# Optimization experiments

Measured on AMD Instinct MI355X. Metric: run time of the kernel, lower is better.

The kernel has to match this reference:

```python
import jax, jax.numpy as jnp
import numpy as np
import math

D = 768      # hidden_size
DK = 128     # d = min(128, hidden)
REL_K = 5
POS_RANGE = 2 * REL_K + 1
SCALING = math.sqrt(2 * DK)
LN_EPS = 1e-5


def setup_inputs() -> dict:
    key = jax.random.key(0)
    ks = jax.random.split(key, 16)
    N, S = 8, 2048
    sequence = jax.random.normal(ks[0], (N, S, D), dtype=jnp.float32)
    attention_mask = jnp.ones((N, S, S), dtype=bool)
    positions = jnp.tile(jnp.arange(S, dtype=jnp.int64)[None, :], (N, 1))
    s = 0.02
    params = dict(
        W_init=jax.random.normal(ks[1], (D, D), jnp.float32) * s,
        b_init=jnp.zeros((D,), jnp.float32),
        ln_g=jnp.ones((D,), jnp.float32),
        ln_b=jnp.zeros((D,), jnp.float32),
        W_u=jax.random.normal(ks[2], (D, 2 * D), jnp.float32) * s,
        b_u=jnp.zeros((2 * D,), jnp.float32),
        W_v=jax.random.normal(ks[3], (D, 2 * D), jnp.float32) * s,
        b_v=jnp.zeros((2 * D,), jnp.float32),
        W_z=jax.random.normal(ks[4], (D, DK), jnp.float32) * s,
        b_z=jnp.zeros((DK,), jnp.float32),
        gamma=jax.random.normal(ks[5], (3, DK), jnp.float32) * 0.02 + 0.0,
        beta=jnp.zeros((3, DK), jnp.float32),
        embed_pos=jax.random.normal(ks[6], (POS_RANGE, DK), jnp.float32),
        W_out=jax.random.normal(ks[7], (2 * D, D), jnp.float32) * s,
        b_out=jnp.zeros((D,), jnp.float32),
        W_gate=jax.random.normal(ks[8], (2 * D, D), jnp.float32) * s,
        b_gate=jnp.zeros((D,), jnp.float32),
    )
    return dict(sequence=sequence, attention_mask=attention_mask, positions=positions, **params)


def _layernorm(x, g, b):
    mu = jnp.mean(x, axis=-1, keepdims=True)
    var = jnp.mean(jnp.square(x - mu), axis=-1, keepdims=True)
    return (x - mu) * jax.lax.rsqrt(var + LN_EPS) * g + b


def reference(sequence, attention_mask, positions,
              W_init, b_init, ln_g, ln_b,
              W_u, b_u, W_v, b_v, W_z, b_z,
              gamma, beta, embed_pos,
              W_out, b_out, W_gate, b_gate):
    res = sequence
    x = _layernorm(sequence @ W_init + b_init, ln_g, ln_b)   # [N,S,D]
    U = jax.nn.silu(x @ W_u + b_u)                            # [N,S,2D]
    V = jax.nn.silu(x @ W_v + b_v)                            # [N,S,2D]
    Z = jax.nn.silu(x @ W_z + b_z)                            # [N,S,dk]
    Q = Z * gamma[0] + beta[0]
    Qp = Z * gamma[1] + beta[1]
    K = Z * gamma[2] + beta[2]
    energy = jnp.einsum('nsd,ntd->nst', Q, K)                 # [N,S,S]
    # relative position bias: Qp projected onto position embeddings,
    # then gathered by clipped relative offset (equivalent to one-hot+sum)
    q_pos = Qp @ embed_pos.T                                  # [N,S,pos_range]
    rel = positions[:, None, :] - positions[:, :, None]       # [N,S,S] = pos_j - pos_i
    rel_idx = jnp.clip(rel, -REL_K, REL_K) + REL_K
    rel_energy = jnp.take_along_axis(q_pos, rel_idx, axis=2)  # [N,S,S]
    logits = (energy + rel_energy) / SCALING
    logits = jnp.where(attention_mask, logits, -jnp.inf)
    attn = jax.nn.softmax(logits, axis=-1)
    V_ = jnp.einsum('nst,ntd->nsd', attn, V)                  # [N,S,2D]
    out = (U * V_) @ W_out + b_out                            # [N,S,D] (dropout inactive at eval)
    gates = jax.nn.sigmoid(jnp.concatenate([out, res], axis=-1) @ W_gate + b_gate)
    out = gates * out + (1.0 - gates) * res
    return out
```

## Files before the change

kernel.cpp:

```cpp
#include <hip/hip_runtime.h>
#include <math.h>


typedef __bf16 bf16x8 __attribute__((ext_vector_type(8)));
typedef float  f32x4  __attribute__((ext_vector_type(4)));

__device__ __forceinline__ float silu_f(float v) { return v / (1.0f + __expf(-v)); }
__device__ __forceinline__ float sigmoid_f(float v) { return 1.0f / (1.0f + __expf(-v)); }

__device__ __forceinline__ unsigned short f2bf(float f) {
    union { float f; unsigned u; } v; v.f = f;
    unsigned r = v.u + 0x7fff + ((v.u >> 16) & 1);
    return (unsigned short)(r >> 16);
}
__device__ __forceinline__ float bf2f(unsigned short h) {
    union { unsigned u; float f; } v; v.u = ((unsigned)h) << 16; return v.f;
}

__device__ __forceinline__ void gload_lds16(const void* g, void* l) {
    __builtin_amdgcn_global_load_lds((const __attribute__((address_space(1))) char*)g,
                                     (__attribute__((address_space(3))) char*)l, 16, 0, 0);
}

template <int EPI, bool DUAL>
__global__ __launch_bounds__(256) void mfma_gemm(
    const unsigned short* __restrict__ A,  int lda, long sA,
    const unsigned short* __restrict__ Bt, int ldb, long sB,
    const unsigned short* __restrict__ A2,
    const unsigned short* __restrict__ Bt2,
    const float* __restrict__ bias,
    const float* __restrict__ aux, long sAux,
    float* __restrict__ aux2,
    void* __restrict__ P0, long sP0,
    void* __restrict__ P1,
    int N, int K)
{
    __shared__ unsigned short As[128 * 64];
    __shared__ unsigned short Bs[128 * 64];
    const int tid  = threadIdx.x;
    const int lane = tid & 63;
    const int wave = tid >> 6;
    const int z    = blockIdx.z;
    const int row0 = blockIdx.y * 128;
    const int col0 = blockIdx.x * 128;

    int c_r[4], c_g[4];
    unsigned short* alp[4];
    unsigned short* blp[4];
#pragma unroll
    for (int ci = 0; ci < 4; ++ci) {
        const int c = ci * 256 + tid;
        const int r = c >> 3;
        c_r[ci] = r;
        c_g[ci] = (c & 7) ^ (r & 7);
        alp[ci] = &As[c * 8];
        blp[ci] = &Bs[c * 8];
    }

    const int wr = (wave >> 1) * 64;
    const int wc = (wave & 1) * 64;
    const int fm  = lane & 15;
    const int kbi = lane >> 4;
    const int er  = kbi * 4;

    int aoff[2][4], boff[2][4];
#pragma unroll
    for (int b = 0; b < 2; ++b)
#pragma unroll
        for (int i = 0; i < 4; ++i) {
            const int r = wr + i * 16 + fm;
            aoff[b][i] = r * 64 + (((b * 4 + kbi) ^ (r & 7)) * 8);
            const int n = wc + i * 16 + fm;
            boff[b][i] = n * 64 + (((b * 4 + kbi) ^ (n & 7)) * 8);
        }

    f32x4 acc[4][4];
#pragma unroll
    for (int i = 0; i < 4; ++i)
#pragma unroll
        for (int j = 0; j < 4; ++j) acc[i][j] = (f32x4){0.f, 0.f, 0.f, 0.f};

    const int npass = DUAL ? 2 : 1;
    for (int pass = 0; pass < npass; ++pass) {
        const unsigned short* Ab = (pass ? A2  : A)  + (size_t)z * sA;
        const unsigned short* Bb = (pass ? Bt2 : Bt) + (size_t)z * sB;
        const unsigned short* ag[4];
        const unsigned short* bg[4];
#pragma unroll
        for (int ci = 0; ci < 4; ++ci) {
            ag[ci] = Ab + (size_t)(row0 + c_r[ci]) * lda + c_g[ci] * 8;
            bg[ci] = Bb + (size_t)(col0 + c_r[ci]) * ldb + c_g[ci] * 8;
        }
        for (int k0 = 0; k0 < K; k0 += 64) {
#pragma unroll
            for (int ci = 0; ci < 4; ++ci) { gload_lds16(ag[ci], alp[ci]); ag[ci] += 64; }
#pragma unroll
            for (int ci = 0; ci < 4; ++ci) { gload_lds16(bg[ci], blp[ci]); bg[ci] += 64; }
            __syncthreads();
#pragma unroll
            for (int b = 0; b < 2; ++b) {
                bf16x8 a[4], bb[4];
#pragma unroll
                for (int i = 0; i < 4; ++i) a[i]  = *(const bf16x8*)&As[aoff[b][i]];
#pragma unroll
                for (int j = 0; j < 4; ++j) bb[j] = *(const bf16x8*)&Bs[boff[b][j]];
#pragma unroll
                for (int i = 0; i < 4; ++i)
#pragma unroll
                    for (int j = 0; j < 4; ++j)
                        acc[i][j] = __builtin_amdgcn_mfma_f32_16x16x32_bf16(
                            a[i], bb[j], acc[i][j], 0, 0, 0);
            }
            __syncthreads();
        }
    }

    if (EPI == 0) {
        unsigned short* Ub = (unsigned short*)P0 + (size_t)z * sP0;
        const float* inv = aux2 + (z << 11);
#pragma unroll
        for (int i = 0; i < 4; ++i)
#pragma unroll
            for (int j = 0; j < 4; ++j) {
                const int m0 = row0 + wr + i * 16 + er;
                const int n  = col0 + wc + j * 16 + fm;
#pragma unroll
                for (int reg = 0; reg < 4; ++reg) {
                    const size_t idx = (size_t)(m0 + reg) * N + n;
                    Ub[idx] = f2bf(acc[i][j][reg] * inv[m0 + reg] * bf2f(Ub[idx]));
                }
            }
    } else if (EPI == 1) {
        const float* qb = aux + (size_t)z * sAux;
        unsigned short* Eb = (unsigned short*)P0 + (size_t)z * sP0;
#pragma unroll
        for (int i = 0; i < 4; ++i) {
            float rs[4] = {0.f, 0.f, 0.f, 0.f};
#pragma unroll
            for (int j = 0; j < 4; ++j) {
                const int n = col0 + wc + j * 16 + fm;
#pragma unroll
                for (int reg = 0; reg < 4; ++reg) {
                    const int m = row0 + wr + i * 16 + er + reg;
                    int d = n - m;
                    d = d < -5 ? -5 : (d > 5 ? 5 : d);
                    const float v =
                        __expf((acc[i][j][reg] + qb[m * 11 + d + 5]) * 0.0625f);
                    const unsigned short h = f2bf(v);
                    Eb[(size_t)m * N + n] = h;
                    rs[reg] += bf2f(h);
                }
            }
#pragma unroll
            for (int reg = 0; reg < 4; ++reg) {
                float s = rs[reg];
                s += __shfl_xor(s, 1); s += __shfl_xor(s, 2);
                s += __shfl_xor(s, 4); s += __shfl_xor(s, 8);
                if (fm == 0) {
                    const int m = row0 + wr + i * 16 + er + reg;
                    aux2[((size_t)(z * 2048 + m)) * 32 + blockIdx.x * 2 + (wave & 1)] = s;
                }
            }
        }
    } else if (EPI == 2) {
        unsigned short* Cb = (unsigned short*)P0;
#pragma unroll
        for (int j = 0; j < 4; ++j) {
            const int n = col0 + wc + j * 16 + fm;
            const float bb = bias[n];
#pragma unroll
            for (int i = 0; i < 4; ++i) {
                const int m0 = row0 + wr + i * 16 + er;
#pragma unroll
                for (int reg = 0; reg < 4; ++reg)
                    Cb[(size_t)(m0 + reg) * N + n] = f2bf(acc[i][j][reg] + bb);
            }
        }
    } else if (EPI == 5) {
        float* Zf = (float*)P0;
#pragma unroll
        for (int j = 0; j < 4; ++j) {
            const int n = col0 + wc + j * 16 + fm;
            const float bb = bias[n];
#pragma unroll
            for (int i = 0; i < 4; ++i) {
                const int m0 = row0 + wr + i * 16 + er;
#pragma unroll
                for (int reg = 0; reg < 4; ++reg)
                    Zf[(size_t)(m0 + reg) * N + n] = silu_f(acc[i][j][reg] + bb);
            }
        }
    } else if (EPI == 6) {
        float* Of = (float*)P0;
        unsigned short* Ob = (unsigned short*)P1;
#pragma unroll
        for (int j = 0; j < 4; ++j) {
            const int n = col0 + wc + j * 16 + fm;
            const float bb = bias[n];
#pragma unroll
            for (int i = 0; i < 4; ++i) {
                const int m0 = row0 + wr + i * 16 + er;
#pragma unroll
                for (int reg = 0; reg < 4; ++reg) {
                    const float v = acc[i][j][reg] + bb;
                    const size_t idx = (size_t)(m0 + reg) * N + n;
                    Of[idx] = v;
                    Ob[idx] = f2bf(v);
                }
            }
        }
    } else if (EPI == 7) {
        float* Of = (float*)P0;
        const float* res = aux;
#pragma unroll
        for (int j = 0; j < 4; ++j) {
            const int n = col0 + wc + j * 16 + fm;
            const float bb = bias[n];
#pragma unroll
            for (int i = 0; i < 4; ++i) {
                const int m0 = row0 + wr + i * 16 + er;
#pragma unroll
                for (int reg = 0; reg < 4; ++reg) {
                    const float g = sigmoid_f(acc[i][j][reg] + bb);
                    const size_t idx = (size_t)(m0 + reg) * N + n;
                    Of[idx] = g * Of[idx] + (1.0f - g) * res[idx];
                }
            }
        }
    } else {
        unsigned short* Ub = (unsigned short*)P0;
        unsigned short* Vt = (unsigned short*)P1;
#pragma unroll
        for (int j = 0; j < 4; ++j) {
            const int n = col0 + wc + j * 16 + fm;
            const bool isU = n < 1536;
            const float bb = isU ? bias[n] : aux2[n - 1536];
#pragma unroll
            for (int i = 0; i < 4; ++i) {
                const int m0 = row0 + wr + i * 16 + er;
                if (isU) {
#pragma unroll
                    for (int reg = 0; reg < 4; ++reg)
                        Ub[(size_t)(m0 + reg) * 1536 + n] =
                            f2bf(silu_f(acc[i][j][reg] + bb));
                } else {
                    const int bat = m0 >> 11;
                    const int sl  = m0 & 2047;
                    unsigned short t[4];
#pragma unroll
                    for (int reg = 0; reg < 4; ++reg)
                        t[reg] = f2bf(silu_f(acc[i][j][reg] + bb));
                    *(ushort4*)(Vt + (size_t)bat * 1536 * 2048
                                + (size_t)(n - 1536) * 2048 + sl) = *(const ushort4*)t;
                }
            }
        }
    }
}

__global__ __launch_bounds__(256) void reduce_inv(
    const float* __restrict__ part, float* __restrict__ inv)
{
    const int r = blockIdx.x * 256 + threadIdx.x;
    const float4* p = (const float4*)(part + (size_t)r * 32);
    float s = 0.f;
#pragma unroll
    for (int k = 0; k < 8; ++k) {
        float4 v = p[k];
        s += v.x + v.y + v.z + v.w;
    }
    inv[r] = 1.0f / s;
}

__global__ __launch_bounds__(256) void transpose_w(
    const float* __restrict__ W, unsigned short* __restrict__ Wt, int K, int N)
{
    __shared__ float t[32][33];
    const int tx = threadIdx.x & 31, ty = threadIdx.x >> 5;
    const int kb = blockIdx.y * 32, nb = blockIdx.x * 32;
#pragma unroll
    for (int r = 0; r < 4; ++r)
        t[ty + 8 * r][tx] = W[(size_t)(kb + ty + 8 * r) * N + nb + tx];
    __syncthreads();
#pragma unroll
    for (int r = 0; r < 4; ++r)
        Wt[(size_t)(nb + ty + 8 * r) * K + kb + tx] = f2bf(t[tx][ty + 8 * r]);
}

__global__ __launch_bounds__(256) void f32_to_bf16(
    const float* __restrict__ in, unsigned short* __restrict__ o)
{
    const size_t i = ((size_t)blockIdx.x * 256 + threadIdx.x) * 4;
    float4 v = *(const float4*)(in + i);
    ushort4 b;
    b.x = f2bf(v.x); b.y = f2bf(v.y); b.z = f2bf(v.z); b.w = f2bf(v.w);
    *(ushort4*)(o + i) = b;
}

__global__ __launch_bounds__(256) void ln_bf16(
    const unsigned short* __restrict__ in, const float* __restrict__ g,
    const float* __restrict__ b, unsigned short* __restrict__ out)
{
    const int row = blockIdx.x;
    const unsigned short* p = in + (size_t)row * 768;
    const int tid = threadIdx.x;
    float v0 = bf2f(p[tid]), v1 = bf2f(p[tid + 256]), v2 = bf2f(p[tid + 512]);
    float s = v0 + v1 + v2;
    float q = v0 * v0 + v1 * v1 + v2 * v2;
#pragma unroll
    for (int off = 32; off; off >>= 1) {
        s += __shfl_xor(s, off);
        q += __shfl_xor(q, off);
    }
    __shared__ float ss[4], qq[4];
    const int wid = tid >> 6, lane = tid & 63;
    if (lane == 0) { ss[wid] = s; qq[wid] = q; }
    __syncthreads();
    s = ss[0] + ss[1] + ss[2] + ss[3];
    q = qq[0] + qq[1] + qq[2] + qq[3];
    const float mu  = s * (1.0f / 768.0f);
    const float var = q * (1.0f / 768.0f) - mu * mu;
    const float inv = rsqrtf(var + 1e-5f);
    unsigned short* o = out + (size_t)row * 768;
    o[tid]       = f2bf((v0 - mu) * inv * g[tid]       + b[tid]);
    o[tid + 256] = f2bf((v1 - mu) * inv * g[tid + 256] + b[tid + 256]);
    o[tid + 512] = f2bf((v2 - mu) * inv * g[tid + 512] + b[tid + 512]);
}

__global__ __launch_bounds__(256) void qpos_kernel(
    const float* __restrict__ Z, const float* __restrict__ g1,
    const float* __restrict__ b1, const float* __restrict__ ep,
    float* __restrict__ qpos)
{
    const int tid = threadIdx.x;
    const int lane = tid & 63;
    const int wid = tid >> 6;
    const int row = blockIdx.x * 4 + wid;
    const float z0 = Z[(size_t)row * 128 + lane];
    const float z1 = Z[(size_t)row * 128 + 64 + lane];
    const float q0 = z0 * g1[lane] + b1[lane];
    const float q1 = z1 * g1[64 + lane] + b1[64 + lane];
#pragma unroll
    for (int p = 0; p < 11; ++p) {
        float s = q0 * ep[p * 128 + lane] + q1 * ep[p * 128 + 64 + lane];
#pragma unroll
        for (int off = 32; off; off >>= 1) s += __shfl_xor(s, off);
        if (lane == 0) qpos[(size_t)row * 11 + p] = s;
    }
}

__global__ __launch_bounds__(256) void qk_affine(
    const float* __restrict__ Z, const float* __restrict__ gamma,
    const float* __restrict__ beta,
    unsigned short* __restrict__ Qb, unsigned short* __restrict__ Kb)
{
    const int idx = blockIdx.x * 256 + threadIdx.x;
    const int row = idx >> 5;
    const int c   = (idx & 31) * 4;
    float4 z  = *(const float4*)(Z + (size_t)row * 128 + c);
    float4 g0 = *(const float4*)(gamma + c);
    float4 B0 = *(const float4*)(beta + c);
    float4 g2 = *(const float4*)(gamma + 256 + c);
    float4 B2 = *(const float4*)(beta + 256 + c);
    ushort4 q, k;
    q.x = f2bf(z.x * g0.x + B0.x); q.y = f2bf(z.y * g0.y + B0.y);
    q.z = f2bf(z.z * g0.z + B0.z); q.w = f2bf(z.w * g0.w + B0.w);
    k.x = f2bf(z.x * g2.x + B2.x); k.y = f2bf(z.y * g2.y + B2.y);
    k.z = f2bf(z.z * g2.z + B2.z); k.w = f2bf(z.w * g2.w + B2.w);
    *(ushort4*)(Qb + (size_t)row * 128 + c) = q;
    *(ushort4*)(Kb + (size_t)row * 128 + c) = k;
}

extern "C" void kernel_launch(void* const* d_in, const int* in_sizes, int n_in,
                              void* d_out, int out_size, void* d_ws, size_t ws_size,
                              hipStream_t stream)
{
    const float* seq    = (const float*)d_in[0];
    const float* W_init = (const float*)d_in[3];
    const float* b_init = (const float*)d_in[4];
    const float* ln_g   = (const float*)d_in[5];
    const float* ln_b   = (const float*)d_in[6];
    const float* W_u    = (const float*)d_in[7];
    const float* b_u    = (const float*)d_in[8];
    const float* W_v    = (const float*)d_in[9];
    const float* b_v    = (const float*)d_in[10];
    const float* W_z    = (const float*)d_in[11];
    const float* b_z    = (const float*)d_in[12];
    const float* gamma  = (const float*)d_in[13];
    const float* beta   = (const float*)d_in[14];
    const float* embed  = (const float*)d_in[15];
    const float* W_out  = (const float*)d_in[16];
    const float* b_out  = (const float*)d_in[17];
    const float* W_gate = (const float*)d_in[18];
    const float* b_gate = (const float*)d_in[19];
    float* out = (float*)d_out;

    char* ws = (char*)d_ws;
    float* Z    = (float*)ws;                     ws += (size_t)16384 * 128 * 4;
    float* qpos = (float*)ws;                     ws += (size_t)16384 * 11 * 4;
    float* part = (float*)ws;                     ws += (size_t)16384 * 32 * 4;
    float* inv  = (float*)ws;                     ws += (size_t)16384 * 4;
    unsigned short* seq_bf = (unsigned short*)ws; ws += (size_t)16384 * 768 * 2;
    unsigned short* G_bf   = (unsigned short*)ws; ws += (size_t)16384 * 768 * 2;
    unsigned short* x_bf   = (unsigned short*)ws; ws += (size_t)16384 * 768 * 2;
    unsigned short* U_bf   = (unsigned short*)ws; ws += (size_t)16384 * 1536 * 2;
    unsigned short* Vt     = (unsigned short*)ws; ws += (size_t)16384 * 1536 * 2;
    unsigned short* out_bf = (unsigned short*)ws; ws += (size_t)16384 * 768 * 2;
    unsigned short* Qb     = (unsigned short*)ws; ws += (size_t)16384 * 128 * 2;
    unsigned short* Kb     = (unsigned short*)ws; ws += (size_t)16384 * 128 * 2;
    unsigned short* E      = (unsigned short*)ws; ws += (size_t)8 * 2048 * 2048 * 2;
    unsigned short* Wit    = (unsigned short*)ws; ws += (size_t)768 * 768 * 2;
    unsigned short* Wuvt   = (unsigned short*)ws; ws += (size_t)3072 * 768 * 2;
    unsigned short* Wzt    = (unsigned short*)ws; ws += (size_t)128 * 768 * 2;
    unsigned short* Wot    = (unsigned short*)ws; ws += (size_t)768 * 1536 * 2;
    unsigned short* Wgt    = (unsigned short*)ws; ws += (size_t)768 * 1536 * 2;

    const dim3 b256(256);

    f32_to_bf16<<<12288, b256, 0, stream>>>(seq, seq_bf);
    transpose_w<<<dim3(24, 24), b256, 0, stream>>>(W_init, Wit, 768, 768);
    transpose_w<<<dim3(48, 24), b256, 0, stream>>>(W_u, Wuvt, 768, 1536);
    transpose_w<<<dim3(48, 24), b256, 0, stream>>>(W_v, Wuvt + (size_t)1536 * 768, 768, 1536);
    transpose_w<<<dim3(4, 24),  b256, 0, stream>>>(W_z, Wzt, 768, 128);
    transpose_w<<<dim3(24, 48), b256, 0, stream>>>(W_out,  Wot, 1536, 768);
    transpose_w<<<dim3(24, 48), b256, 0, stream>>>(W_gate, Wgt, 1536, 768);

    mfma_gemm<2, false><<<dim3(6, 128), b256, 0, stream>>>(
        seq_bf, 768, 0, Wit, 768, 0, nullptr, nullptr,
        b_init, nullptr, 0, nullptr, G_bf, 0, nullptr, 768, 768);
    ln_bf16<<<16384, b256, 0, stream>>>(G_bf, ln_g, ln_b, x_bf);
    mfma_gemm<8, false><<<dim3(24, 128), b256, 0, stream>>>(
        x_bf, 768, 0, Wuvt, 768, 0, nullptr, nullptr,
        b_u, nullptr, 0, (float*)b_v, U_bf, 0, Vt, 3072, 768);
    mfma_gemm<5, false><<<dim3(1, 128), b256, 0, stream>>>(
        x_bf, 768, 0, Wzt, 768, 0, nullptr, nullptr,
        b_z, nullptr, 0, nullptr, Z, 0, nullptr, 128, 768);
    qpos_kernel<<<4096, b256, 0, stream>>>(Z, gamma + 128, beta + 128, embed, qpos);
    qk_affine<<<2048, b256, 0, stream>>>(Z, gamma, beta, Qb, Kb);

    mfma_gemm<1, false><<<dim3(16, 16, 8), b256, 0, stream>>>(
        Qb, 128, 2048L * 128, Kb, 128, 2048L * 128,
        nullptr, nullptr, nullptr,
        qpos, 2048L * 11, part,
        E, 2048L * 2048, nullptr, 2048, 128);
    reduce_inv<<<64, b256, 0, stream>>>(part, inv);
    mfma_gemm<0, false><<<dim3(12, 16, 8), b256, 0, stream>>>(
        E, 2048, 2048L * 2048, Vt, 2048, 1536L * 2048,
        nullptr, nullptr, nullptr, nullptr, 0, inv,
        U_bf, 2048L * 1536, nullptr, 1536, 2048);

    mfma_gemm<6, false><<<dim3(6, 128), b256, 0, stream>>>(
        U_bf, 1536, 0, Wot, 1536, 0, nullptr, nullptr,
        b_out, nullptr, 0, nullptr, out, 0, out_bf, 768, 1536);
    mfma_gemm<7, true><<<dim3(6, 128), b256, 0, stream>>>(
        out_bf, 768, 0, Wgt, 1536, 0, seq_bf, Wgt + 768,
        b_gate, seq, 0, nullptr, out, 0, nullptr, 768, 768);
}
```

Before: 880.7 us.

## Add 256x256-tile 8-wave GEMM with interleaved LDS staging for large GEMMs

Introduces a new gemm256 kernel with 512 threads, 256x256 output tiles, a K-step of 128 split into two double-buffered 64-wide halves, and direct global-to-LDS loads. Loads are interleaved with MFMA quadrants under explicit waitcnt/barrier control and s_setprio. The init, UV, attention-times-V, out and gate GEMMs move to it, while the QK and Z GEMMs stay on the old 128-tile kernel. The larger tiles raise data reuse per LDS byte and hide load latency, at the cost of 128 KB of LDS, more accumulator registers, fewer blocks per GPU, and fragile hand-written synchronisation.

Result: slower. 947.4 us (+7.6%).

```diff
diff --git a/kernel.cpp b/kernel.cpp
--- a/kernel.cpp
+++ b/kernel.cpp
@@ -115,22 +115,7 @@
         }
     }
 
-    if (EPI == 0) {
-        unsigned short* Ub = (unsigned short*)P0 + (size_t)z * sP0;
-        const float* inv = aux2 + (z << 11);
-#pragma unroll
-        for (int i = 0; i < 4; ++i)
-#pragma unroll
-            for (int j = 0; j < 4; ++j) {
-                const int m0 = row0 + wr + i * 16 + er;
-                const int n  = col0 + wc + j * 16 + fm;
-#pragma unroll
-                for (int reg = 0; reg < 4; ++reg) {
-                    const size_t idx = (size_t)(m0 + reg) * N + n;
-                    Ub[idx] = f2bf(acc[i][j][reg] * inv[m0 + reg] * bf2f(Ub[idx]));
-                }
-            }
-    } else if (EPI == 1) {
+    if (EPI == 1) {
         const float* qb = aux + (size_t)z * sAux;
         unsigned short* Eb = (unsigned short*)P0 + (size_t)z * sP0;
 #pragma unroll
@@ -162,8 +147,8 @@
                 }
             }
         }
-    } else if (EPI == 2) {
-        unsigned short* Cb = (unsigned short*)P0;
+    } else if (EPI == 5) {
+        float* Zf = (float*)P0;
 #pragma unroll
         for (int j = 0; j < 4; ++j) {
             const int n = col0 + wc + j * 16 + fm;
@@ -173,21 +158,192 @@
                 const int m0 = row0 + wr + i * 16 + er;
 #pragma unroll
                 for (int reg = 0; reg < 4; ++reg)
-                    Cb[(size_t)(m0 + reg) * N + n] = f2bf(acc[i][j][reg] + bb);
-            }
-        }
-    } else if (EPI == 5) {
-        float* Zf = (float*)P0;
+                    Zf[(size_t)(m0 + reg) * N + n] = silu_f(acc[i][j][reg] + bb);
+            }
+        }
+    }
+}
+
+#define BAR()  __builtin_amdgcn_s_barrier()
+#define LGK0() asm volatile("s_waitcnt lgkmcnt(0)")
+#define LGK8() asm volatile("s_waitcnt lgkmcnt(8)")
+#define VMC4() asm volatile("s_waitcnt vmcnt(4)")
+#define VMC0() asm volatile("s_waitcnt vmcnt(0)")
+
+template <int EPI, bool DUAL>
+__global__ __launch_bounds__(512, 2) void gemm256(
+    const unsigned short* __restrict__ A,  int lda, long sA,
+    const unsigned short* __restrict__ Bt, int ldb, long sB,
+    const unsigned short* __restrict__ A2,
+    const float* __restrict__ bias,
+    const float* __restrict__ aux,
+    float* __restrict__ aux2,
+    void* __restrict__ P0, long sP0,
+    void* __restrict__ P1,
+    int N, int K, int ntA)
+{
+    __shared__ unsigned short As[2][16384];
+    __shared__ unsigned short Bs[2][16384];
+    const int tid  = threadIdx.x;
+    const int lane = tid & 63;
+    const int wave = tid >> 6;
+    const int z    = blockIdx.z;
+    const int row0 = blockIdx.y * 256;
+    const int col0 = blockIdx.x * 256;
+
+    const int wr  = (wave >> 2) * 128;
+    const int wc  = (wave & 3) * 64;
+    const int fm  = lane & 15;
+    const int kbi = lane >> 4;
+    const int er  = kbi * 4;
+
+    const int sw0  = (kbi ^ (fm & 7)) * 8;
+    const int sw1  = ((4 + kbi) ^ (fm & 7)) * 8;
+    const int aof0 = (wr + fm) * 64 + sw0;
+    const int aof1 = (wr + fm) * 64 + sw1;
+    const int bof0 = (wc + fm) * 64 + sw0;
+    const int bof1 = (wc + fm) * 64 + sw1;
+
+    const int r0s = tid >> 3;
+    const int g0  = ((tid & 7) ^ (r0s & 7)) * 8;
+    const int r1s = r0s + 64;
+    const int g1  = ((tid & 7) ^ (r1s & 7)) * 8;
+    const int l0  = tid * 8;
+    const int l1  = tid * 8 + 4096;
+
+    const unsigned short* Abase = A  + (size_t)z * sA + (size_t)row0 * lda;
+    const unsigned short* Bbase = Bt + (size_t)z * sB + (size_t)col0 * ldb;
+
+#define STAGE_A(buf, h, t) do {                                               \
+    const unsigned short* _p;                                                 \
+    if (!DUAL || (t) < ntA) _p = Abase + (size_t)((h) * 128) * lda + (t) * 64;\
+    else _p = A2 + (size_t)(row0 + (h) * 128) * lda + ((t) - ntA) * 64;       \
+    gload_lds16(_p + (size_t)r0s * lda + g0, &As[buf][(h) * 8192 + l0]);      \
+    gload_lds16(_p + (size_t)r1s * lda + g1, &As[buf][(h) * 8192 + l1]);      \
+} while (0)
+
+#define STAGE_B(buf, h, t) do {                                               \
+    const unsigned short* _p = Bbase + (size_t)((h) * 128) * ldb + (t) * 64;  \
+    gload_lds16(_p + (size_t)r0s * ldb + g0, &Bs[buf][(h) * 8192 + l0]);      \
+    gload_lds16(_p + (size_t)r1s * ldb + g1, &Bs[buf][(h) * 8192 + l1]);      \
+} while (0)
+
+#define LD_A(buf, MH) do {                                                    \
+    _Pragma("unroll") for (int f = 0; f < 4; ++f) {                           \
+        Aq[0][f] = *(const bf16x8*)&As[buf][aof0 + ((MH) * 4 + f) * 1024];    \
+        Aq[1][f] = *(const bf16x8*)&As[buf][aof1 + ((MH) * 4 + f) * 1024];    \
+    } } while (0)
+
+#define LD_B(buf, NH) do {                                                    \
+    _Pragma("unroll") for (int g = 0; g < 2; ++g) {                           \
+        Bq[NH][0][g] = *(const bf16x8*)&Bs[buf][bof0 + ((NH) * 2 + g) * 1024];\
+        Bq[NH][1][g] = *(const bf16x8*)&Bs[buf][bof1 + ((NH) * 2 + g) * 1024];\
+    } } while (0)
+
+#define MFMA_Q(MH, NH) do {                                                   \
+    __builtin_amdgcn_s_setprio(1);                                            \
+    _Pragma("unroll") for (int kb = 0; kb < 2; ++kb)                          \
+    _Pragma("unroll") for (int f = 0; f < 4; ++f)                             \
+    _Pragma("unroll") for (int g = 0; g < 2; ++g)                             \
+        acc[(MH) * 4 + f][(NH) * 2 + g] =                                     \
+            __builtin_amdgcn_mfma_f32_16x16x32_bf16(                          \
+                Aq[kb][f], Bq[NH][kb][g], acc[(MH) * 4 + f][(NH) * 2 + g],    \
+                0, 0, 0);                                                     \
+    __builtin_amdgcn_s_setprio(0);                                            \
+} while (0)
+
+    bf16x8 Aq[2][4];
+    bf16x8 Bq[2][2][2];
+    f32x4  acc[8][4];
+#pragma unroll
+    for (int i = 0; i < 8; ++i)
+#pragma unroll
+        for (int j = 0; j < 4; ++j) acc[i][j] = (f32x4){0.f, 0.f, 0.f, 0.f};
+
+    const int nit = K >> 7;
+
+    STAGE_A(0, 0, 0); STAGE_A(0, 1, 0);
+    STAGE_B(0, 0, 0); STAGE_B(0, 1, 0);
+    STAGE_B(1, 0, 1); STAGE_B(1, 1, 1);
+    VMC4();
+    BAR();
+
+    for (int i = 0; i < nit; ++i) {
+        const bool more = (i + 1 < nit);
+        const int t1 = 2 * i + 1, t2 = 2 * i + 2, t3 = 2 * i + 3;
+        LD_A(0, 0); LD_B(0, 0);
+        STAGE_A(1, 0, t1);
+        LGK8(); BAR(); LGK0();
+        MFMA_Q(0, 0);
+        BAR();
+        LD_B(0, 1);
+        STAGE_A(1, 1, t1);
+        BAR(); LGK0();
+        MFMA_Q(0, 1);
+        BAR();
+        LD_A(0, 1);
+        if (more) STAGE_B(0, 0, t2);
+        BAR(); LGK0();
+        MFMA_Q(1, 1);
+        BAR();
+        if (more) { STAGE_B(0, 1, t2); VMC4(); } else { VMC0(); }
+        BAR();
+        MFMA_Q(1, 0);
+        BAR();
+        LD_A(1, 0); LD_B(1, 0);
+        if (more) STAGE_A(0, 0, t2);
+        LGK8(); BAR(); LGK0();
+        MFMA_Q(0, 0);
+        BAR();
+        LD_B(1, 1);
+        if (more) STAGE_A(0, 1, t2);
+        BAR(); LGK0();
+        MFMA_Q(0, 1);
+        BAR();
+        LD_A(1, 1);
+        if (more) STAGE_B(1, 0, t3);
+        BAR(); LGK0();
+        MFMA_Q(1, 1);
+        BAR();
+        if (more) { STAGE_B(1, 1, t3); VMC4(); }
+        BAR();
+        MFMA_Q(1, 0);
+        BAR();
+    }
+
+#undef STAGE_A
+#undef STAGE_B
+#undef LD_A
+#undef LD_B
+#undef MFMA_Q
+
+    if (EPI == 0) {
+        unsigned short* Ub = (unsigned short*)P0 + (size_t)z * sP0;
+        const float* inv = aux2 + (z << 11);
+#pragma unroll
+        for (int i = 0; i < 8; ++i)
+#pragma unroll
+            for (int j = 0; j < 4; ++j) {
+                const int m0 = row0 + wr + i * 16 + er;
+                const int n  = col0 + wc + j * 16 + fm;
+#pragma unroll
+                for (int reg = 0; reg < 4; ++reg) {
+                    const size_t idx = (size_t)(m0 + reg) * N + n;
+                    Ub[idx] = f2bf(acc[i][j][reg] * inv[m0 + reg] * bf2f(Ub[idx]));
+                }
+            }
+    } else if (EPI == 2) {
+        unsigned short* Cb = (unsigned short*)P0;
 #pragma unroll
         for (int j = 0; j < 4; ++j) {
             const int n = col0 + wc + j * 16 + fm;
             const float bb = bias[n];
 #pragma unroll
-            for (int i = 0; i < 4; ++i) {
+            for (int i = 0; i < 8; ++i) {
                 const int m0 = row0 + wr + i * 16 + er;
 #pragma unroll
                 for (int reg = 0; reg < 4; ++reg)
-                    Zf[(size_t)(m0 + reg) * N + n] = silu_f(acc[i][j][reg] + bb);
+                    Cb[(size_t)(m0 + reg) * N + n] = f2bf(acc[i][j][reg] + bb);
             }
         }
     } else if (EPI == 6) {
@@ -198,7 +354,7 @@
             const int n = col0 + wc + j * 16 + fm;
             const float bb = bias[n];
 #pragma unroll
-            for (int i = 0; i < 4; ++i) {
+            for (int i = 0; i < 8; ++i) {
                 const int m0 = row0 + wr + i * 16 + er;
 #pragma unroll
                 for (int reg = 0; reg < 4; ++reg) {
@@ -217,7 +373,7 @@
             const int n = col0 + wc + j * 16 + fm;
             const float bb = bias[n];
 #pragma unroll
-            for (int i = 0; i < 4; ++i) {
+            for (int i = 0; i < 8; ++i) {
                 const int m0 = row0 + wr + i * 16 + er;
 #pragma unroll
                 for (int reg = 0; reg < 4; ++reg) {
@@ -227,7 +383,7 @@
                 }
             }
         }
-    } else {
+    } else if (EPI == 8) {
         unsigned short* Ub = (unsigned short*)P0;
         unsigned short* Vt = (unsigned short*)P1;
 #pragma unroll
@@ -236,7 +392,7 @@
             const bool isU = n < 1536;
             const float bb = isU ? bias[n] : aux2[n - 1536];
 #pragma unroll
-            for (int i = 0; i < 4; ++i) {
+            for (int i = 0; i < 8; ++i) {
                 const int m0 = row0 + wr + i * 16 + er;
                 if (isU) {
 #pragma unroll
@@ -416,6 +572,7 @@
     unsigned short* Wgt    = (unsigned short*)ws; ws += (size_t)768 * 1536 * 2;
 
     const dim3 b256(256);
+    const dim3 b512(512);
 
     f32_to_bf16<<<12288, b256, 0, stream>>>(seq, seq_bf);
     transpose_w<<<dim3(24, 24), b256, 0, stream>>>(W_init, Wit, 768, 768);
@@ -425,13 +582,13 @@
     transpose_w<<<dim3(24, 48), b256, 0, stream>>>(W_out,  Wot, 1536, 768);
     transpose_w<<<dim3(24, 48), b256, 0, stream>>>(W_gate, Wgt, 1536, 768);
 
-    mfma_gemm<2, false><<<dim3(6, 128), b256, 0, stream>>>(
-        seq_bf, 768, 0, Wit, 768, 0, nullptr, nullptr,
-        b_init, nullptr, 0, nullptr, G_bf, 0, nullptr, 768, 768);
+    gemm256<2, false><<<dim3(3, 64), b512, 0, stream>>>(
+        seq_bf, 768, 0, Wit, 768, 0, nullptr,
+        b_init, nullptr, nullptr, G_bf, 0, nullptr, 768, 768, 0);
     ln_bf16<<<16384, b256, 0, stream>>>(G_bf, ln_g, ln_b, x_bf);
-    mfma_gemm<8, false><<<dim3(24, 128), b256, 0, stream>>>(
-        x_bf, 768, 0, Wuvt, 768, 0, nullptr, nullptr,
-        b_u, nullptr, 0, (float*)b_v, U_bf, 0, Vt, 3072, 768);
+    gemm256<8, false><<<dim3(12, 64), b512, 0, stream>>>(
+        x_bf, 768, 0, Wuvt, 768, 0, nullptr,
+        b_u, nullptr, (float*)b_v, U_bf, 0, Vt, 3072, 768, 0);
     mfma_gemm<5, false><<<dim3(1, 128), b256, 0, stream>>>(
         x_bf, 768, 0, Wzt, 768, 0, nullptr, nullptr,
         b_z, nullptr, 0, nullptr, Z, 0, nullptr, 128, 768);
@@ -444,15 +601,14 @@
         qpos, 2048L * 11, part,
         E, 2048L * 2048, nullptr, 2048, 128);
     reduce_inv<<<64, b256, 0, stream>>>(part, inv);
-    mfma_gemm<0, false><<<dim3(12, 16, 8), b256, 0, stream>>>(
-        E, 2048, 2048L * 2048, Vt, 2048, 1536L * 2048,
-        nullptr, nullptr, nullptr, nullptr, 0, inv,
-        U_bf, 2048L * 1536, nullptr, 1536, 2048);
-
-    mfma_gemm<6, false><<<dim3(6, 128), b256, 0, stream>>>(
-        U_bf, 1536, 0, Wot, 1536, 0, nullptr, nullptr,
-        b_out, nullptr, 0, nullptr, out, 0, out_bf, 768, 1536);
-    mfma_gemm<7, true><<<dim3(6, 128), b256, 0, stream>>>(
-        out_bf, 768, 0, Wgt, 1536, 0, seq_bf, Wgt + 768,
-        b_gate, seq, 0, nullptr, out, 0, nullptr, 768, 768);
-}
+    gemm256<0, false><<<dim3(6, 8, 8), b512, 0, stream>>>(
+        E, 2048, 2048L * 2048, Vt, 2048, 1536L * 2048, nullptr,
+        nullptr, nullptr, inv, U_bf, 2048L * 1536, nullptr, 1536, 2048, 0);
+
+    gemm256<6, false><<<dim3(3, 64), b512, 0, stream>>>(
+        U_bf, 1536, 0, Wot, 1536, 0, nullptr,
+        b_out, nullptr, nullptr, out, 0, out_bf, 768, 1536, 0);
+    gemm256<7, true><<<dim3(3, 64), b512, 0, stream>>>(
+        out_bf, 768, 0, Wgt, 1536, 0, seq_bf,
+        b_gate, seq, nullptr, out, 0, nullptr, 768, 1536, 12);
+}
```
